# Kernel tuning notes

Hardware: AMD Instinct MI355X
Metric: run time of the kernel (lower is better)

Reference implementation:

```python
import jax, jax.numpy as jnp
import numpy as np

B, N, D, H = 4, 256, 32, 512

def setup_inputs() -> dict:
    key = jax.random.key(0)
    ks = jax.random.split(key, 6)
    z = jax.random.normal(ks[0], (B, N, D), dtype=jnp.float32)
    motif_mask = (jax.random.uniform(ks[1], (B, N)) > 0.5).astype(jnp.float32)
    residue_mask = jnp.ones((B, N), dtype=jnp.float32)
    # Linear weights stored as (in, out); scaled like torch default init
    W1 = jax.random.normal(ks[2], (D * D, H), dtype=jnp.float32) / np.sqrt(D * D)
    b1 = jnp.zeros((H,), dtype=jnp.float32)
    W2 = jax.random.normal(ks[3], (H, H // 2), dtype=jnp.float32) / np.sqrt(H)
    b2 = jnp.zeros((H // 2,), dtype=jnp.float32)
    W3 = jax.random.normal(ks[4], (H // 2, 1), dtype=jnp.float32) / np.sqrt(H // 2)
    b3 = jnp.zeros((1,), dtype=jnp.float32)
    return {"z": z, "motif_mask": motif_mask, "residue_mask": residue_mask,
            "W1": W1, "b1": b1, "W2": W2, "b2": b2, "W3": W3, "b3": b3}

def reference(z, motif_mask, residue_mask, W1, b1, W2, b2, W3, b3):
    # kron[b,i,j, a*D+c] = z[b,i,a] * z[b,j,c]; first Linear on kron is the
    # bilinear form z_i^T W1_h z_j -- compute via two matmuls, never
    # materializing the (B,N,N,D^2) tensor.
    d = z.shape[-1]
    W1r = W1.reshape(d, d, -1)                      # (D, D, H); axis0 = z_i dim, axis1 = z_j dim
    tmp = jnp.einsum('bia,ach->bihc', z, W1r)        # (B, N, H, D)
    h1 = jax.nn.relu(jnp.einsum('bihc,bjc->bijh', tmp, z) + b1)  # (B, N, N, H)
    h2 = jax.nn.relu(jnp.einsum('bijh,hk->bijk', h1, W2) + b2)   # (B, N, N, H/2)
    contact_logits = (jnp.einsum('bijk,ko->bijo', h2, W3) + b3)[..., 0]  # (B, N, N)
    outer_mask = motif_mask[:, None, :] * motif_mask[:, :, None]
    contact_logits = contact_logits * outer_mask
    contact_map = jax.nn.sigmoid(contact_logits)
    return (contact_map, contact_logits)
```

## Files before the change

### kernel.cpp

```cpp
#include <hip/hip_runtime.h>
#include <hip/hip_bf16.h>
#include <cstdint>
#include <cstddef>

#define NB 4
#define NN 256
#define DD 32
#define HH 512

typedef __attribute__((ext_vector_type(8))) short short8;
typedef __attribute__((ext_vector_type(4))) float f32x4;
typedef __attribute__((ext_vector_type(16))) float f32x16;

static __device__ __forceinline__ unsigned cvtpk(float a, float b) {
  unsigned r;
  asm("v_cvt_pk_bf16_f32 %0, %1, %2" : "=v"(r) : "v"(a), "v"(b));
  return r;
}
static __device__ __forceinline__ unsigned short f2bf1(float a) {
  return (unsigned short)(cvtpk(a, 0.f) & 0xffffu);
}

static __device__ __forceinline__ short8 pack8(float4 a0, float4 a1) {
  union { unsigned u[4]; short8 s; } r;
  r.u[0] = cvtpk(a0.x, a0.y); r.u[1] = cvtpk(a0.z, a0.w);
  r.u[2] = cvtpk(a1.x, a1.y); r.u[3] = cvtpk(a1.z, a1.w);
  return r.s;
}

__global__ __launch_bounds__(256) void prep(const float* __restrict__ z,
                                            const float* __restrict__ W1,
                                            const float* __restrict__ W2,
                                            const float* __restrict__ motif,
                                            unsigned short* __restrict__ W2F,
                                            unsigned short* __restrict__ Tall,
                                            int* __restrict__ jlist,
                                            int* __restrict__ jcnt,
                                            int* __restrict__ wq,
                                            int* __restrict__ wqn,
                                            float* __restrict__ out) {
  const int blk = blockIdx.x;
  const int tid = threadIdx.x;
  if (blk < 512) {
    __shared__ unsigned short w1s[16384];
    const int nblk = blk >> 4, mgrp = blk & 15;
    const int bibase = mgrp * 64;

    #pragma unroll
    for (int r = 0; r < 16; ++r) {
      int task = r * 256 + tid;
      int row = task >> 2;
      int hq = task & 3;
      float4 v = *(const float4*)(W1 + (size_t)row * 512 + nblk * 16 + hq * 4);
      int a = row >> 5, c = row & 31;
      int quad = a >> 3, e = a & 7;
      float hv[4] = {v.x, v.y, v.z, v.w};
      #pragma unroll
      for (int vv = 0; vv < 4; ++vv) {
        int hl = hq * 4 + vv;
        int nl = hl * 32 + c;
        int w2 = nl >> 7, r7 = nl & 127;
        int l16 = r7 >> 3, nt = r7 & 7;
        w1s[((w2 * 8 + nt) * 64 + quad * 16 + l16) * 8 + e] = f2bf1(hv[vv]);
      }
    }
    __syncthreads();

    const int w2 = tid >> 6, lane = tid & 63;
    const int quad = lane >> 4, l16 = lane & 15;

    short8 bfr[8];
    #pragma unroll
    for (int nt = 0; nt < 8; ++nt)
      bfr[nt] = *(const short8*)&w1s[((w2 * 8 + nt) * 64 + lane) * 8];

    const int ncol = nblk * 512 + w2 * 128 + l16 * 8;
    #pragma unroll
    for (int mtg = 0; mtg < 2; ++mtg) {
      short8 afr[2];
      #pragma unroll
      for (int mi = 0; mi < 2; ++mi) {
        const float* zr = z + (size_t)(bibase + (mtg * 2 + mi) * 16 + l16) * 32 + quad * 8;
        float4 a0 = *(const float4*)(zr);
        float4 a1 = *(const float4*)(zr + 4);
        afr[mi] = pack8(a0, a1);
      }
      f32x4 d[2][8];
      #pragma unroll
      for (int mi = 0; mi < 2; ++mi)
        #pragma unroll
        for (int nt = 0; nt < 8; ++nt)
          d[mi][nt] = __builtin_amdgcn_mfma_f32_16x16x32_bf16(
              afr[mi], bfr[nt], (f32x4){0.f, 0.f, 0.f, 0.f}, 0, 0, 0);
      #pragma unroll
      for (int mi = 0; mi < 2; ++mi)
        #pragma unroll
        for (int r = 0; r < 4; ++r) {
          size_t rowoff = (size_t)(bibase + (mtg * 2 + mi) * 16 + quad * 4 + r) * 16384;
          uint4 p;
          p.x = cvtpk(d[mi][0][r], d[mi][1][r]);
          p.y = cvtpk(d[mi][2][r], d[mi][3][r]);
          p.z = cvtpk(d[mi][4][r], d[mi][5][r]);
          p.w = cvtpk(d[mi][6][r], d[mi][7][r]);
          *(uint4*)&Tall[rowoff + ncol] = p;
        }
    }
  } else if (blk < 576) {
    int f8 = (blk - 512) * 256 + tid;
    int lane = f8 & 63;
    int nt = (f8 >> 6) & 1, s = (f8 >> 7) & 3, hc = (f8 >> 9) & 7, w = (f8 >> 12) & 3;
    int k2 = w * 64 + nt * 32 + (lane & 31);
    int hb = hc * 64 + s * 16 + (lane >> 5) * 8;
    float v[8];
    #pragma unroll
    for (int e = 0; e < 8; ++e) v[e] = W2[(hb + e) * 256 + k2];
    uint4 p;
    p.x = cvtpk(v[0], v[1]); p.y = cvtpk(v[2], v[3]);
    p.z = cvtpk(v[4], v[5]); p.w = cvtpk(v[6], v[7]);
    ((uint4*)W2F)[f8] = p;
  } else if (blk == 576) {
    __shared__ int itemc[4];
    __shared__ int baseh[4];
    const int w = tid >> 6, lane = tid & 63;
    int cnt = 0;
    if (w < NB) {
      #pragma unroll
      for (int ch = 0; ch < 4; ++ch) {
        int j = ch * 64 + lane;
        float m = motif[w * 256 + j];
        bool alive = (m != 0.f);
        unsigned long long mk = __ballot(alive);
        unsigned long long below = mk & ((1ull << lane) - 1ull);
        int pos = __popcll(below);
        if (alive) jlist[w * 256 + cnt + pos] = j;
        cnt += __popcll(mk);
      }
      if (lane == 0) {
        jcnt[w] = cnt;
        itemc[w] = cnt * ((cnt + 63) >> 6);
      }
    }
    __syncthreads();
    if (tid == 0) {
      int s = 0;
      #pragma unroll
      for (int k = 0; k < NB; ++k) { baseh[k] = s; s += itemc[k]; }
      *wqn = s;
    }
    __syncthreads();
    if (w < NB) {
      const int K = (cnt + 63) >> 6;
      const int base = baseh[w];
      int rank = 0;
      #pragma unroll
      for (int ch = 0; ch < 4; ++ch) {
        int i = ch * 64 + lane;
        bool alive = (motif[w * 256 + i] != 0.f);
        unsigned long long mk = __ballot(alive);
        unsigned long long below = mk & ((1ull << lane) - 1ull);
        int pos = __popcll(below);
        if (alive)
          for (int jt = 0; jt < K; ++jt)
            wq[base + (rank + pos) * K + jt] = (w * 256 + i) * 4 + jt;
        rank += __popcll(mk);
      }
    }
  } else {
    const size_t OUT2 = (size_t)NB * NN * NN;
    int t0 = (blk - 577) * 256 + tid;
    #pragma unroll
    for (int k = 0; k < 4; ++k) {
      int p = t0 + k * 65536;
      int bi = p >> 8, j = p & 255, b = bi >> 8;
      bool masked = (motif[bi] == 0.f) || (motif[b * 256 + j] == 0.f);
      if (masked) {
        out[p] = 0.5f;
        out[OUT2 + p] = 0.f;
      }
    }
  }
}

__global__ __launch_bounds__(256) void fused(const unsigned short* __restrict__ Tall,
                                             const unsigned short* __restrict__ W2F,
                                             const float* __restrict__ z,
                                             const float* __restrict__ b1,
                                             const float* __restrict__ b2,
                                             const float* __restrict__ W3,
                                             const float* __restrict__ b3,
                                             const float* __restrict__ motif,
                                             const int* __restrict__ jlist,
                                             const int* __restrict__ jcnt,
                                             const int* __restrict__ wq,
                                             const int* __restrict__ wqn,
                                             float* __restrict__ out) {
  __shared__ unsigned short h1s[64 * 264];
  __shared__ float red[256];

  const int bx = blockIdx.x;
  if (bx >= *wqn) return;
  const int item = wq[bx];

  const int tid = threadIdx.x;
  const int w = tid >> 6, lane = tid & 63;
  const int quad = lane >> 4, l16 = lane & 15;
  const int L = lane >> 5, c32 = lane & 31;
  const size_t OUT2 = (size_t)NB * NN * NN;

  const int bi = item >> 2, jt = item & 3;
  const int b = bi >> 8;
  const int cnt = jcnt[b];
  const int slotbase = jt * 64;
  const float mi_v = motif[bi];

  short8 zfr[4];
  #pragma unroll
  for (int nt = 0; nt < 4; ++nt) {
    int slot = slotbase + nt * 16 + l16;
    int sc = slot < cnt ? slot : cnt - 1;
    int jj = jlist[b * 256 + sc] & 255;
    const float* zr = z + (size_t)(b * 256 + jj) * 32 + quad * 8;
    float4 a0 = *(const float4*)(zr);
    float4 a1 = *(const float4*)(zr + 4);
    zfr[nt] = pack8(a0, a1);
  }

  float b2v[2], w3v[2];
  #pragma unroll
  for (int nt = 0; nt < 2; ++nt) {
    int k2 = w * 64 + nt * 32 + c32;
    b2v[nt] = b2[k2];
    w3v[nt] = W3[k2];
  }

  f32x16 acc[2][2];
  #pragma unroll
  for (int mt = 0; mt < 2; ++mt)
    #pragma unroll
    for (int nt = 0; nt < 2; ++nt)
      acc[mt][nt] = (f32x16){0.f,0.f,0.f,0.f,0.f,0.f,0.f,0.f,
                             0.f,0.f,0.f,0.f,0.f,0.f,0.f,0.f};

  const unsigned short* Tbase = Tall + (size_t)bi * 16384 + (w * 16 + l16) * 32 + quad * 8;
  const unsigned short* Wp = W2F + w * 32768 + lane * 8;
  const float* b1base = b1 + w * 16 + quad * 4;

  #pragma unroll
  for (int half = 0; half < 2; ++half) {
    short8 tfr[4];
    #pragma unroll
    for (int q = 0; q < 4; ++q)
      tfr[q] = *(const short8*)(Tbase + (half * 4 + q) * 2048);
    #pragma unroll
    for (int q = 0; q < 4; ++q) {
      float4 b1f = *(const float4*)(b1base + (half * 4 + q) * 64);
      f32x4 cin = {b1f.x, b1f.y, b1f.z, b1f.w};
      #pragma unroll
      for (int nt = 0; nt < 4; ++nt) {
        f32x4 d = __builtin_amdgcn_mfma_f32_16x16x32_bf16(tfr[q], zfr[nt], cin, 0, 0, 0);
        uint2 p;
        p.x = cvtpk(fmaxf(d[0], 0.f), fmaxf(d[1], 0.f));
        p.y = cvtpk(fmaxf(d[2], 0.f), fmaxf(d[3], 0.f));
        *(uint2*)&h1s[(nt * 16 + l16) * 264 + q * 64 + w * 16 + quad * 4] = p;
      }
    }
    __syncthreads();

    const unsigned short* Wh = Wp + half * 16384;
    const unsigned short* h1r = &h1s[c32 * 264 + L * 8];
    short8 bfp[3][2], afp[2][2];
    #pragma unroll
    for (int p = 0; p < 3; ++p) {
      bfp[p][0] = *(const short8*)(Wh + p * 1024);
      bfp[p][1] = *(const short8*)(Wh + p * 1024 + 512);
    }
    afp[0][0] = *(const short8*)(h1r);
    afp[0][1] = *(const short8*)(h1r + 32 * 264);
    afp[1][0] = *(const short8*)(h1r + 16);
    afp[1][1] = *(const short8*)(h1r + 32 * 264 + 16);
    #pragma unroll
    for (int u = 0; u < 16; ++u) {
      const int cur = u & 1, bq = u % 3;
      short8 a0 = afp[cur][0], a1 = afp[cur][1];
      short8 b0 = bfp[bq][0], b1q = bfp[bq][1];
      if (u < 14) {
        afp[cur][0] = *(const short8*)(h1r + (u + 2) * 16);
        afp[cur][1] = *(const short8*)(h1r + 32 * 264 + (u + 2) * 16);
      }
      if (u < 13) {
        bfp[bq][0] = *(const short8*)(Wh + (u + 3) * 1024);
        bfp[bq][1] = *(const short8*)(Wh + (u + 3) * 1024 + 512);
      }
      acc[0][0] = __builtin_amdgcn_mfma_f32_32x32x16_bf16(a0, b0, acc[0][0], 0, 0, 0);
      acc[0][1] = __builtin_amdgcn_mfma_f32_32x32x16_bf16(a0, b1q, acc[0][1], 0, 0, 0);
      acc[1][0] = __builtin_amdgcn_mfma_f32_32x32x16_bf16(a1, b0, acc[1][0], 0, 0, 0);
      acc[1][1] = __builtin_amdgcn_mfma_f32_32x32x16_bf16(a1, b1q, acc[1][1], 0, 0, 0);
    }
    if (half == 0) __syncthreads();
  }

  float pr[2][16];
  #pragma unroll
  for (int mt = 0; mt < 2; ++mt)
    #pragma unroll
    for (int reg = 0; reg < 16; ++reg) {
      float s = 0.f;
      #pragma unroll
      for (int nt = 0; nt < 2; ++nt) {
        float v = acc[mt][nt][reg] + b2v[nt];
        v = v > 0.f ? v : 0.f;
        s += v * w3v[nt];
      }
      s += __shfl_xor(s, 1);
      s += __shfl_xor(s, 2);
      s += __shfl_xor(s, 4);
      s += __shfl_xor(s, 8);
      s += __shfl_xor(s, 16);
      pr[mt][reg] = s;
    }
  if (c32 == 0) {
    #pragma unroll
    for (int mt = 0; mt < 2; ++mt)
      #pragma unroll
      for (int g = 0; g < 4; ++g) {
        float4 vv = {pr[mt][g * 4 + 0], pr[mt][g * 4 + 1],
                     pr[mt][g * 4 + 2], pr[mt][g * 4 + 3]};
        *(float4*)&red[w * 64 + mt * 32 + g * 8 + L * 4] = vv;
      }
  }
  __syncthreads();
  if (tid < 64) {
    int slot = slotbase + tid;
    if (slot < cnt) {
      int j = jlist[b * 256 + slot] & 255;
      float logit = red[tid] + red[64 + tid] + red[128 + tid] + red[192 + tid] + b3[0];
      float mm = mi_v * motif[b * 256 + j];
      logit *= mm;
      float map = 1.f / (1.f + expf(-logit));
      size_t idx = (size_t)bi * 256 + j;
      out[idx] = map;
      out[OUT2 + idx] = logit;
    }
  }
}

extern "C" void kernel_launch(void* const* d_in, const int* in_sizes, int n_in,
                              void* d_out, int out_size, void* d_ws, size_t ws_size,
                              hipStream_t stream) {
  const float* z     = (const float*)d_in[0];
  const float* motif = (const float*)d_in[1];
  const float* W1 = (const float*)d_in[3];
  const float* b1 = (const float*)d_in[4];
  const float* W2 = (const float*)d_in[5];
  const float* b2 = (const float*)d_in[6];
  const float* W3 = (const float*)d_in[7];
  const float* b3 = (const float*)d_in[8];
  float* out = (float*)d_out;

  char* ws = (char*)d_ws;
  unsigned short* Tall = (unsigned short*)ws;
  unsigned short* W2F  = (unsigned short*)(ws + 33554432);
  int* jlist = (int*)(ws + 33554432 + 262144);
  int* jcnt  = (int*)(ws + 33554432 + 262144 + 4096);
  int* wq    = (int*)(ws + 33554432 + 262144 + 4096 + 64);
  int* wqn   = (int*)(ws + 33554432 + 262144 + 4096 + 64 + 16384);

  prep<<<833, 256, 0, stream>>>(z, W1, W2, motif, W2F, Tall,
                                jlist, jcnt, wq, wqn, out);
  fused<<<4096, 256, 0, stream>>>(Tall, W2F, z, b1, b2, W3, b3, motif,
                                  jlist, jcnt, wq, wqn, out);
}
```

Measured before the change: 125.7 us.

## Split fused block into 8 waves over j-halves and skip masked T rows

```diff
diff --git a/kernel.cpp b/kernel.cpp
--- a/kernel.cpp
+++ b/kernel.cpp
@@ -96,13 +96,15 @@
       for (int mi = 0; mi < 2; ++mi)
         #pragma unroll
         for (int r = 0; r < 4; ++r) {
-          size_t rowoff = (size_t)(bibase + (mtg * 2 + mi) * 16 + quad * 4 + r) * 16384;
-          uint4 p;
-          p.x = cvtpk(d[mi][0][r], d[mi][1][r]);
-          p.y = cvtpk(d[mi][2][r], d[mi][3][r]);
-          p.z = cvtpk(d[mi][4][r], d[mi][5][r]);
-          p.w = cvtpk(d[mi][6][r], d[mi][7][r]);
-          *(uint4*)&Tall[rowoff + ncol] = p;
+          int rowbi = bibase + (mtg * 2 + mi) * 16 + quad * 4 + r;
+          if (motif[rowbi] != 0.f) {
+            uint4 p;
+            p.x = cvtpk(d[mi][0][r], d[mi][1][r]);
+            p.y = cvtpk(d[mi][2][r], d[mi][3][r]);
+            p.z = cvtpk(d[mi][4][r], d[mi][5][r]);
+            p.w = cvtpk(d[mi][6][r], d[mi][7][r]);
+            *(uint4*)&Tall[(size_t)rowbi * 16384 + ncol] = p;
+          }
         }
     }
   } else if (blk < 576) {
@@ -181,7 +183,7 @@
   }
 }
 
-__global__ __launch_bounds__(256) void fused(const unsigned short* __restrict__ Tall,
+__global__ __launch_bounds__(512) void fused(const unsigned short* __restrict__ Tall,
                                              const unsigned short* __restrict__ W2F,
                                              const float* __restrict__ z,
                                              const float* __restrict__ b1,
@@ -202,9 +204,10 @@
   const int item = wq[bx];
 
   const int tid = threadIdx.x;
-  const int w = tid >> 6, lane = tid & 63;
+  const int w8 = tid >> 6, lane = tid & 63;
   const int quad = lane >> 4, l16 = lane & 15;
   const int L = lane >> 5, c32 = lane & 31;
+  const int w = w8 & 3, jh = w8 >> 2;
   const size_t OUT2 = (size_t)NB * NN * NN;
 
   const int bi = item >> 2, jt = item & 3;
@@ -233,27 +236,25 @@
     w3v[nt] = W3[k2];
   }
 
-  f32x16 acc[2][2];
-  #pragma unroll
-  for (int mt = 0; mt < 2; ++mt)
-    #pragma unroll
-    for (int nt = 0; nt < 2; ++nt)
-      acc[mt][nt] = (f32x16){0.f,0.f,0.f,0.f,0.f,0.f,0.f,0.f,
-                             0.f,0.f,0.f,0.f,0.f,0.f,0.f,0.f};
-
-  const unsigned short* Tbase = Tall + (size_t)bi * 16384 + (w * 16 + l16) * 32 + quad * 8;
+  f32x16 acc[2];
+  #pragma unroll
+  for (int nt = 0; nt < 2; ++nt)
+    acc[nt] = (f32x16){0.f,0.f,0.f,0.f,0.f,0.f,0.f,0.f,
+                       0.f,0.f,0.f,0.f,0.f,0.f,0.f,0.f};
+
+  const unsigned short* Tbase = Tall + (size_t)bi * 16384 + (w8 * 16 + l16) * 32 + quad * 8;
   const unsigned short* Wp = W2F + w * 32768 + lane * 8;
-  const float* b1base = b1 + w * 16 + quad * 4;
+  const float* b1base = b1 + w8 * 16 + quad * 4;
 
   #pragma unroll
   for (int half = 0; half < 2; ++half) {
-    short8 tfr[4];
-    #pragma unroll
-    for (int q = 0; q < 4; ++q)
-      tfr[q] = *(const short8*)(Tbase + (half * 4 + q) * 2048);
-    #pragma unroll
-    for (int q = 0; q < 4; ++q) {
-      float4 b1f = *(const float4*)(b1base + (half * 4 + q) * 64);
+    short8 tfr[2];
+    #pragma unroll
+    for (int q = 0; q < 2; ++q)
+      tfr[q] = *(const short8*)(Tbase + half * 8192 + q * 4096);
+    #pragma unroll
+    for (int q = 0; q < 2; ++q) {
+      float4 b1f = *(const float4*)(b1base + half * 256 + q * 128);
       f32x4 cin = {b1f.x, b1f.y, b1f.z, b1f.w};
       #pragma unroll
       for (int nt = 0; nt < 4; ++nt) {
@@ -261,72 +262,61 @@
         uint2 p;
         p.x = cvtpk(fmaxf(d[0], 0.f), fmaxf(d[1], 0.f));
         p.y = cvtpk(fmaxf(d[2], 0.f), fmaxf(d[3], 0.f));
-        *(uint2*)&h1s[(nt * 16 + l16) * 264 + q * 64 + w * 16 + quad * 4] = p;
+        *(uint2*)&h1s[(nt * 16 + l16) * 264 + q * 128 + w8 * 16 + quad * 4] = p;
       }
     }
     __syncthreads();
 
     const unsigned short* Wh = Wp + half * 16384;
-    const unsigned short* h1r = &h1s[c32 * 264 + L * 8];
-    short8 bfp[3][2], afp[2][2];
+    const unsigned short* h1r = &h1s[(jh * 32 + c32) * 264 + L * 8];
+    short8 bfp[3][2], afp[2];
     #pragma unroll
     for (int p = 0; p < 3; ++p) {
       bfp[p][0] = *(const short8*)(Wh + p * 1024);
       bfp[p][1] = *(const short8*)(Wh + p * 1024 + 512);
     }
-    afp[0][0] = *(const short8*)(h1r);
-    afp[0][1] = *(const short8*)(h1r + 32 * 264);
-    afp[1][0] = *(const short8*)(h1r + 16);
-    afp[1][1] = *(const short8*)(h1r + 32 * 264 + 16);
+    afp[0] = *(const short8*)(h1r);
+    afp[1] = *(const short8*)(h1r + 16);
     #pragma unroll
     for (int u = 0; u < 16; ++u) {
       const int cur = u & 1, bq = u % 3;
-      short8 a0 = afp[cur][0], a1 = afp[cur][1];
+      short8 a0 = afp[cur];
       short8 b0 = bfp[bq][0], b1q = bfp[bq][1];
-      if (u < 14) {
-        afp[cur][0] = *(const short8*)(h1r + (u + 2) * 16);
-        afp[cur][1] = *(const short8*)(h1r + 32 * 264 + (u + 2) * 16);
-      }
+      if (u < 14)
+        afp[cur] = *(const short8*)(h1r + (u + 2) * 16);
       if (u < 13) {
         bfp[bq][0] = *(const short8*)(Wh + (u + 3) * 1024);
         bfp[bq][1] = *(const short8*)(Wh + (u + 3) * 1024 + 512);
       }
-      acc[0][0] = __builtin_amdgcn_mfma_f32_32x32x16_bf16(a0, b0, acc[0][0], 0, 0, 0);
-      acc[0][1] = __builtin_amdgcn_mfma_f32_32x32x16_bf16(a0, b1q, acc[0][1], 0, 0, 0);
-      acc[1][0] = __builtin_amdgcn_mfma_f32_32x32x16_bf16(a1, b0, acc[1][0], 0, 0, 0);
-      acc[1][1] = __builtin_amdgcn_mfma_f32_32x32x16_bf16(a1, b1q, acc[1][1], 0, 0, 0);
+      acc[0] = __builtin_amdgcn_mfma_f32_32x32x16_bf16(a0, b0, acc[0], 0, 0, 0);
+      acc[1] = __builtin_amdgcn_mfma_f32_32x32x16_bf16(a0, b1q, acc[1], 0, 0, 0);
     }
     if (half == 0) __syncthreads();
   }
 
-  float pr[2][16];
-  #pragma unroll
-  for (int mt = 0; mt < 2; ++mt)
-    #pragma unroll
-    for (int reg = 0; reg < 16; ++reg) {
-      float s = 0.f;
-      #pragma unroll
-      for (int nt = 0; nt < 2; ++nt) {
-        float v = acc[mt][nt][reg] + b2v[nt];
-        v = v > 0.f ? v : 0.f;
-        s += v * w3v[nt];
-      }
-      s += __shfl_xor(s, 1);
-      s += __shfl_xor(s, 2);
-      s += __shfl_xor(s, 4);
-      s += __shfl_xor(s, 8);
-      s += __shfl_xor(s, 16);
-      pr[mt][reg] = s;
-    }
+  float pr[16];
+  #pragma unroll
+  for (int reg = 0; reg < 16; ++reg) {
+    float s = 0.f;
+    #pragma unroll
+    for (int nt = 0; nt < 2; ++nt) {
+      float v = acc[nt][reg] + b2v[nt];
+      v = v > 0.f ? v : 0.f;
+      s += v * w3v[nt];
+    }
+    s += __shfl_xor(s, 1);
+    s += __shfl_xor(s, 2);
+    s += __shfl_xor(s, 4);
+    s += __shfl_xor(s, 8);
+    s += __shfl_xor(s, 16);
+    pr[reg] = s;
+  }
   if (c32 == 0) {
     #pragma unroll
-    for (int mt = 0; mt < 2; ++mt)
-      #pragma unroll
-      for (int g = 0; g < 4; ++g) {
-        float4 vv = {pr[mt][g * 4 + 0], pr[mt][g * 4 + 1],
-                     pr[mt][g * 4 + 2], pr[mt][g * 4 + 3]};
-        *(float4*)&red[w * 64 + mt * 32 + g * 8 + L * 4] = vv;
-      }
+    for (int g = 0; g < 4; ++g) {
+      float4 vv = {pr[g * 4 + 0], pr[g * 4 + 1], pr[g * 4 + 2], pr[g * 4 + 3]};
+      *(float4*)&red[w * 64 + jh * 32 + g * 8 + L * 4] = vv;
+    }
   }
   __syncthreads();
   if (tid < 64) {
@@ -367,6 +357,6 @@
 
   prep<<<833, 256, 0, stream>>>(z, W1, W2, motif, W2F, Tall,
                                 jlist, jcnt, wq, wqn, out);
-  fused<<<4096, 256, 0, stream>>>(Tall, W2F, z, b1, b2, W3, b3, motif,
+  fused<<<4096, 512, 0, stream>>>(Tall, W2F, z, b1, b2, W3, b3, motif,
                                   jlist, jcnt, wq, wqn, out);
 }
```

Measured after the change: 141.0 us. 12.2% more time.

## Skip Tall writes for masked rows and move mask fill into idle fused blocks

Applied to the files above, without the earlier changes.

```diff
diff --git a/kernel.cpp b/kernel.cpp
--- a/kernel.cpp
+++ b/kernel.cpp
@@ -37,8 +37,7 @@
                                             int* __restrict__ jlist,
                                             int* __restrict__ jcnt,
                                             int* __restrict__ wq,
-                                            int* __restrict__ wqn,
-                                            float* __restrict__ out) {
+                                            int* __restrict__ wqn) {
   const int blk = blockIdx.x;
   const int tid = threadIdx.x;
   if (blk < 512) {
@@ -96,13 +95,15 @@
       for (int mi = 0; mi < 2; ++mi)
         #pragma unroll
         for (int r = 0; r < 4; ++r) {
-          size_t rowoff = (size_t)(bibase + (mtg * 2 + mi) * 16 + quad * 4 + r) * 16384;
-          uint4 p;
-          p.x = cvtpk(d[mi][0][r], d[mi][1][r]);
-          p.y = cvtpk(d[mi][2][r], d[mi][3][r]);
-          p.z = cvtpk(d[mi][4][r], d[mi][5][r]);
-          p.w = cvtpk(d[mi][6][r], d[mi][7][r]);
-          *(uint4*)&Tall[rowoff + ncol] = p;
+          int rowbi = bibase + (mtg * 2 + mi) * 16 + quad * 4 + r;
+          if (motif[rowbi] != 0.f) {
+            uint4 p;
+            p.x = cvtpk(d[mi][0][r], d[mi][1][r]);
+            p.y = cvtpk(d[mi][2][r], d[mi][3][r]);
+            p.z = cvtpk(d[mi][4][r], d[mi][5][r]);
+            p.w = cvtpk(d[mi][6][r], d[mi][7][r]);
+            *(uint4*)&Tall[(size_t)rowbi * 16384 + ncol] = p;
+          }
         }
     }
   } else if (blk < 576) {
@@ -118,7 +119,7 @@
     p.x = cvtpk(v[0], v[1]); p.y = cvtpk(v[2], v[3]);
     p.z = cvtpk(v[4], v[5]); p.w = cvtpk(v[6], v[7]);
     ((uint4*)W2F)[f8] = p;
-  } else if (blk == 576) {
+  } else {
     __shared__ int itemc[4];
     __shared__ int baseh[4];
     const int w = tid >> 6, lane = tid & 63;
@@ -163,19 +164,6 @@
           for (int jt = 0; jt < K; ++jt)
             wq[base + (rank + pos) * K + jt] = (w * 256 + i) * 4 + jt;
         rank += __popcll(mk);
-      }
-    }
-  } else {
-    const size_t OUT2 = (size_t)NB * NN * NN;
-    int t0 = (blk - 577) * 256 + tid;
-    #pragma unroll
-    for (int k = 0; k < 4; ++k) {
-      int p = t0 + k * 65536;
-      int bi = p >> 8, j = p & 255, b = bi >> 8;
-      bool masked = (motif[bi] == 0.f) || (motif[b * 256 + j] == 0.f);
-      if (masked) {
-        out[p] = 0.5f;
-        out[OUT2 + p] = 0.f;
       }
     }
   }
@@ -198,20 +186,38 @@
   __shared__ float red[256];
 
   const int bx = blockIdx.x;
-  if (bx >= *wqn) return;
+  const int tid = threadIdx.x;
+  const size_t OUT2 = (size_t)NB * NN * NN;
+  const int nq = *wqn;
+
+  if (bx >= nq) {
+    const int nf = (int)gridDim.x - nq;
+    for (int p = (bx - nq) * 256 + tid; p < NB * NN * NN; p += nf * 256) {
+      int bi = p >> 8, j = p & 255, b = bi >> 8;
+      if (motif[bi] == 0.f || motif[b * 256 + j] == 0.f) {
+        out[p] = 0.5f;
+        out[OUT2 + p] = 0.f;
+      }
+    }
+    return;
+  }
   const int item = wq[bx];
 
-  const int tid = threadIdx.x;
   const int w = tid >> 6, lane = tid & 63;
   const int quad = lane >> 4, l16 = lane & 15;
   const int L = lane >> 5, c32 = lane & 31;
-  const size_t OUT2 = (size_t)NB * NN * NN;
 
   const int bi = item >> 2, jt = item & 3;
   const int b = bi >> 8;
   const int cnt = jcnt[b];
   const int slotbase = jt * 64;
   const float mi_v = motif[bi];
+
+  const unsigned short* Tbase = Tall + (size_t)bi * 16384 + (w * 16 + l16) * 32 + quad * 8;
+  short8 tfr[8];
+  #pragma unroll
+  for (int q = 0; q < 8; ++q)
+    tfr[q] = *(const short8*)(Tbase + q * 2048);
 
   short8 zfr[4];
   #pragma unroll
@@ -241,23 +247,19 @@
       acc[mt][nt] = (f32x16){0.f,0.f,0.f,0.f,0.f,0.f,0.f,0.f,
                              0.f,0.f,0.f,0.f,0.f,0.f,0.f,0.f};
 
-  const unsigned short* Tbase = Tall + (size_t)bi * 16384 + (w * 16 + l16) * 32 + quad * 8;
   const unsigned short* Wp = W2F + w * 32768 + lane * 8;
   const float* b1base = b1 + w * 16 + quad * 4;
 
   #pragma unroll
   for (int half = 0; half < 2; ++half) {
-    short8 tfr[4];
-    #pragma unroll
-    for (int q = 0; q < 4; ++q)
-      tfr[q] = *(const short8*)(Tbase + (half * 4 + q) * 2048);
     #pragma unroll
     for (int q = 0; q < 4; ++q) {
       float4 b1f = *(const float4*)(b1base + (half * 4 + q) * 64);
       f32x4 cin = {b1f.x, b1f.y, b1f.z, b1f.w};
       #pragma unroll
       for (int nt = 0; nt < 4; ++nt) {
-        f32x4 d = __builtin_amdgcn_mfma_f32_16x16x32_bf16(tfr[q], zfr[nt], cin, 0, 0, 0);
+        f32x4 d = __builtin_amdgcn_mfma_f32_16x16x32_bf16(
+            tfr[half * 4 + q], zfr[nt], cin, 0, 0, 0);
         uint2 p;
         p.x = cvtpk(fmaxf(d[0], 0.f), fmaxf(d[1], 0.f));
         p.y = cvtpk(fmaxf(d[2], 0.f), fmaxf(d[3], 0.f));
@@ -365,8 +367,8 @@
   int* wq    = (int*)(ws + 33554432 + 262144 + 4096 + 64);
   int* wqn   = (int*)(ws + 33554432 + 262144 + 4096 + 64 + 16384);
 
-  prep<<<833, 256, 0, stream>>>(z, W1, W2, motif, W2F, Tall,
-                                jlist, jcnt, wq, wqn, out);
+  prep<<<577, 256, 0, stream>>>(z, W1, W2, motif, W2F, Tall,
+                                jlist, jcnt, wq, wqn);
   fused<<<4096, 256, 0, stream>>>(Tall, W2F, z, b1, b2, W3, b3, motif,
                                   jlist, jcnt, wq, wqn, out);
 }
```

Result: no change. 125.1 us (-0.5%).
